# Optimization experiments

Measured on AMD Instinct MI355X. Metric: run time of the kernel, lower is better.

## Reference

```python
import jax, jax.numpy as jnp
import numpy as np

N_NODES = 100000
N_EDGES = 3200000
IN_F, HID_F, OUT_F = 6, 32, 3


def setup_inputs() -> dict:
    key = jax.random.key(0)
    k_feat, k_src, k_dst, k_w1, k_w2 = jax.random.split(key, 5)
    features = jax.random.normal(k_feat, (N_NODES, IN_F), dtype=jnp.float32)
    src = jax.random.randint(k_src, (N_EDGES,), 0, N_NODES, dtype=jnp.int32)
    dst = jax.random.randint(k_dst, (N_EDGES,), 0, N_NODES, dtype=jnp.int32)
    # Glorot-style weights for the two customConv layers
    W1 = jax.random.normal(k_w1, (IN_F, HID_F), dtype=jnp.float32) / np.sqrt(IN_F)
    b1 = jnp.zeros((HID_F,), dtype=jnp.float32)
    W2 = jax.random.normal(k_w2, (HID_F, OUT_F), dtype=jnp.float32) / np.sqrt(HID_F)
    b2 = jnp.zeros((OUT_F,), dtype=jnp.float32)
    return {"features": features, "src": src, "dst": dst,
            "W1": W1, "b1": b1, "W2": W2, "b2": b2}


def _custom_conv(src, dst, h, W, b):
    """DGL-GraphConv-style layer: mean-aggregate src->dst, then linear.
    h: [N, F_in]; returns [N, F_out]."""
    n = h.shape[0]
    # gather source features along edges, scatter-add to destinations
    msg_sum = jax.ops.segment_sum(h[src], dst, num_segments=n)  # [N, F_in]
    deg = jax.ops.segment_sum(jnp.ones_like(dst, dtype=h.dtype), dst,
                              num_segments=n)                    # [N]
    agg = msg_sum / jnp.maximum(deg, 1.0)[:, None]               # mean over in-neighbors
    return agg @ W + b


def reference(features, src, dst, W1, b1, W2, b2):
    x = _custom_conv(src, dst, features, W1, b1)  # [N, 32]
    x = jax.nn.relu(x)                            # activation inside customConv
    x = _custom_conv(src, dst, x, W2, b2)         # [N, 3]
    return x
```

## Files before the change

### kernel.cpp

```cpp
#include <hip/hip_runtime.h>


#define IN_F 6
#define HID_F 32
#define OUT_F 3

#define NPB 256
#define NPB_SHIFT 8
#define NBMAX 512
#define CAPB 9728
#define CHUNK 8192
#define SRC_BITS 17
#define SRC_MASK ((1u << SRC_BITS) - 1)

__global__ __launch_bounds__(1024)
void k_scatter(const int* __restrict__ src, const int* __restrict__ dst,
               int nB, int* __restrict__ cursor_g,
               unsigned* __restrict__ packed, int nE) {
    __shared__ int      hist[NBMAX];
    __shared__ int      base_l[NBMAX];
    __shared__ int      base_g[NBMAX];
    __shared__ int      cur[NBMAX];
    __shared__ unsigned sorted_l[CHUNK];
    __shared__ unsigned short bkt_l[CHUNK];

    const int tid = threadIdx.x;
    int e0 = blockIdx.x * CHUNK;
    int e1 = min(e0 + CHUNK, nE);
    int cnt = e1 - e0;

    for (int b = tid; b < nB; b += blockDim.x) hist[b] = 0;
    __syncthreads();

    for (int e = e0 + tid; e < e1; e += blockDim.x)
        atomicAdd(&hist[dst[e] >> NPB_SHIFT], 1);
    __syncthreads();

    if (tid < nB) base_l[tid] = hist[tid];
    __syncthreads();
    for (int off = 1; off < nB; off <<= 1) {
        int v = 0;
        if (tid < nB) {
            v = base_l[tid];
            if (tid >= off) v += base_l[tid - off];
        }
        __syncthreads();
        if (tid < nB) base_l[tid] = v;
        __syncthreads();
    }

    int h_r = 0, ex_r = 0;
    if (tid < nB) {
        h_r  = hist[tid];
        ex_r = base_l[tid] - h_r;
        base_g[tid] = h_r ? atomicAdd(&cursor_g[tid], h_r) : 0;
        cur[tid] = ex_r;
    }
    __syncthreads();
    if (tid < nB) base_l[tid] = ex_r;
    __syncthreads();

    for (int e = e0 + tid; e < e1; e += blockDim.x) {
        int d = dst[e];
        int b = d >> NPB_SHIFT;
        unsigned rec = ((unsigned)(d & (NPB - 1)) << SRC_BITS) | (unsigned)src[e];
        int p = atomicAdd(&cur[b], 1);
        sorted_l[p] = rec;
        bkt_l[p] = (unsigned short)b;
    }
    __syncthreads();

    for (int i = tid; i < cnt; i += blockDim.x) {
        int b = bkt_l[i];
        int rel = base_g[b] + (i - base_l[b]);
        if (rel < CAPB) packed[(size_t)b * CAPB + rel] = sorted_l[i];
    }
}

__global__ __launch_bounds__(1024)
void k_sort(unsigned* __restrict__ packed, const int* __restrict__ cursor_g,
            int* __restrict__ offv, int* __restrict__ cntv, int nN) {
    __shared__ int      hist[NPB];
    __shared__ int      base[NPB];
    __shared__ int      cur[NPB];
    __shared__ unsigned sorted[CAPB];

    const int tid = threadIdx.x;
    int b = blockIdx.x;
    int ecnt = min(cursor_g[b], CAPB);
    unsigned* ep = packed + (size_t)b * CAPB;

    if (tid < NPB) hist[tid] = 0;
    __syncthreads();

    for (int i = tid; i < ecnt; i += blockDim.x)
        atomicAdd(&hist[ep[i] >> SRC_BITS], 1);
    __syncthreads();

    if (tid < NPB) base[tid] = hist[tid];
    __syncthreads();
    for (int off = 1; off < NPB; off <<= 1) {
        int v = 0;
        if (tid < NPB) {
            v = base[tid];
            if (tid >= off) v += base[tid - off];
        }
        __syncthreads();
        if (tid < NPB) base[tid] = v;
        __syncthreads();
    }

    int n0 = b << NPB_SHIFT;
    int h_r = 0, ex_r = 0;
    if (tid < NPB) {
        h_r  = hist[tid];
        ex_r = base[tid] - h_r;
        cur[tid] = ex_r;
        int n = n0 + tid;
        if (n < nN) { offv[n] = b * CAPB + ex_r; cntv[n] = h_r; }
    }
    __syncthreads();
    if (tid < NPB) base[tid] = ex_r;
    __syncthreads();

    for (int i = tid; i < ecnt; i += blockDim.x) {
        unsigned p = ep[i];
        int dl = (int)(p >> SRC_BITS);
        int pos = atomicAdd(&cur[dl], 1);
        sorted[pos] = p & SRC_MASK;
    }
    __syncthreads();

    for (int i = tid; i < ecnt; i += blockDim.x) ep[i] = sorted[i];
}

__global__ void k_l1(const unsigned* __restrict__ csr, const int* __restrict__ offv,
                     const int* __restrict__ cntv, const float* __restrict__ feat,
                     const float* __restrict__ W1, const float* __restrict__ b1,
                     const float* __restrict__ W2, float4* __restrict__ g4, int nN) {
    __shared__ float sW1[IN_F * HID_F];
    __shared__ float sb1[HID_F];
    __shared__ float sW2[HID_F * OUT_F];
    for (int i = threadIdx.x; i < IN_F * HID_F; i += blockDim.x)  sW1[i] = W1[i];
    for (int i = threadIdx.x; i < HID_F; i += blockDim.x)         sb1[i] = b1[i];
    for (int i = threadIdx.x; i < HID_F * OUT_F; i += blockDim.x) sW2[i] = W2[i];
    __syncthreads();

    int n = blockIdx.x * blockDim.x + threadIdx.x;
    if (n >= nN) return;

    int off = offv[n], c = cntv[n];
    const unsigned* row = csr + off;

    float s0 = 0.f, s1 = 0.f, s2 = 0.f, s3 = 0.f, s4 = 0.f, s5 = 0.f;
#define ACC_FEAT(S)                                                        \
    do {                                                                   \
        const float* f = feat + (size_t)(S) * IN_F;                        \
        float2 f01 = *reinterpret_cast<const float2*>(f + 0);              \
        float2 f23 = *reinterpret_cast<const float2*>(f + 2);              \
        float2 f45 = *reinterpret_cast<const float2*>(f + 4);              \
        s0 += f01.x; s1 += f01.y; s2 += f23.x;                             \
        s3 += f23.y; s4 += f45.x; s5 += f45.y;                             \
    } while (0)

    int i = 0;
    for (; i + 4 <= c; i += 4) {
        unsigned a0 = row[i], a1 = row[i + 1], a2 = row[i + 2], a3 = row[i + 3];
        ACC_FEAT(a0); ACC_FEAT(a1); ACC_FEAT(a2); ACC_FEAT(a3);
    }
    for (; i < c; ++i) ACC_FEAT(row[i]);
#undef ACC_FEAT

    float inv = 1.0f / fmaxf((float)c, 1.0f);
    float a0 = s0 * inv, a1 = s1 * inv, a2 = s2 * inv;
    float a3 = s3 * inv, a4 = s4 * inv, a5 = s5 * inv;

    float g0 = 0.f, g1 = 0.f, g2 = 0.f;
#pragma unroll
    for (int j = 0; j < HID_F; ++j) {
        float t = sb1[j];
        t = fmaf(a0, sW1[0 * HID_F + j], t);
        t = fmaf(a1, sW1[1 * HID_F + j], t);
        t = fmaf(a2, sW1[2 * HID_F + j], t);
        t = fmaf(a3, sW1[3 * HID_F + j], t);
        t = fmaf(a4, sW1[4 * HID_F + j], t);
        t = fmaf(a5, sW1[5 * HID_F + j], t);
        t = fmaxf(t, 0.0f);
        g0 = fmaf(t, sW2[j * OUT_F + 0], g0);
        g1 = fmaf(t, sW2[j * OUT_F + 1], g1);
        g2 = fmaf(t, sW2[j * OUT_F + 2], g2);
    }
    g4[n] = make_float4(g0, g1, g2, 0.0f);
}

__global__ void k_l2(const unsigned* __restrict__ csr, const int* __restrict__ offv,
                     const int* __restrict__ cntv, const float4* __restrict__ g4,
                     const float* __restrict__ b2, float* __restrict__ out, int nN) {
    int n = blockIdx.x * blockDim.x + threadIdx.x;
    if (n >= nN) return;

    int off = offv[n], c = cntv[n];
    const unsigned* row = csr + off;

    float s0 = 0.f, s1 = 0.f, s2 = 0.f;
    int i = 0;
    for (; i + 4 <= c; i += 4) {
        unsigned a0 = row[i], a1 = row[i + 1], a2 = row[i + 2], a3 = row[i + 3];
        float4 ga = g4[a0], gb = g4[a1], gc = g4[a2], gd = g4[a3];
        s0 += ga.x + gb.x + gc.x + gd.x;
        s1 += ga.y + gb.y + gc.y + gd.y;
        s2 += ga.z + gb.z + gc.z + gd.z;
    }
    for (; i < c; ++i) {
        float4 ga = g4[row[i]];
        s0 += ga.x; s1 += ga.y; s2 += ga.z;
    }

    float inv = 1.0f / fmaxf((float)c, 1.0f);
    out[(size_t)n * OUT_F + 0] = s0 * inv + b2[0];
    out[(size_t)n * OUT_F + 1] = s1 * inv + b2[1];
    out[(size_t)n * OUT_F + 2] = s2 * inv + b2[2];
}

__global__ void scatter1(const int* __restrict__ src, const int* __restrict__ dst,
                         const float* __restrict__ feat,
                         float* __restrict__ acc1, float* __restrict__ deg, int nE) {
    int e = blockIdx.x * blockDim.x + threadIdx.x;
    if (e >= nE) return;
    int s = src[e], d = dst[e];
    const float* f = feat + (size_t)s * IN_F;
    float* a = acc1 + (size_t)d * IN_F;
    float2 f01 = *reinterpret_cast<const float2*>(f + 0);
    float2 f23 = *reinterpret_cast<const float2*>(f + 2);
    float2 f45 = *reinterpret_cast<const float2*>(f + 4);
    atomicAdd(a + 0, f01.x); atomicAdd(a + 1, f01.y); atomicAdd(a + 2, f23.x);
    atomicAdd(a + 3, f23.y); atomicAdd(a + 4, f45.x); atomicAdd(a + 5, f45.y);
    atomicAdd(deg + d, 1.0f);
}

__global__ void node_mlp(float* __restrict__ acc1, const float* __restrict__ deg,
                         const float* __restrict__ W1, const float* __restrict__ b1,
                         const float* __restrict__ W2, int nN) {
    __shared__ float sW1[IN_F * HID_F];
    __shared__ float sb1[HID_F];
    __shared__ float sW2[HID_F * OUT_F];
    for (int i = threadIdx.x; i < IN_F * HID_F; i += blockDim.x)  sW1[i] = W1[i];
    for (int i = threadIdx.x; i < HID_F; i += blockDim.x)         sb1[i] = b1[i];
    for (int i = threadIdx.x; i < HID_F * OUT_F; i += blockDim.x) sW2[i] = W2[i];
    __syncthreads();
    int n = blockIdx.x * blockDim.x + threadIdx.x;
    if (n >= nN) return;
    float inv = 1.0f / fmaxf(deg[n], 1.0f);
    float a[IN_F];
    float* row = acc1 + (size_t)n * IN_F;
#pragma unroll
    for (int i = 0; i < IN_F; ++i) a[i] = row[i] * inv;
    float g0 = 0.f, g1 = 0.f, g2 = 0.f;
#pragma unroll
    for (int j = 0; j < HID_F; ++j) {
        float t = sb1[j];
#pragma unroll
        for (int i = 0; i < IN_F; ++i) t = fmaf(a[i], sW1[i * HID_F + j], t);
        t = fmaxf(t, 0.0f);
        g0 = fmaf(t, sW2[j * OUT_F + 0], g0);
        g1 = fmaf(t, sW2[j * OUT_F + 1], g1);
        g2 = fmaf(t, sW2[j * OUT_F + 2], g2);
    }
    row[0] = g0; row[1] = g1; row[2] = g2;
}

__global__ void scatter2(const int* __restrict__ src, const int* __restrict__ dst,
                         const float* __restrict__ g, float* __restrict__ acc2, int nE) {
    int e = blockIdx.x * blockDim.x + threadIdx.x;
    if (e >= nE) return;
    int s = src[e], d = dst[e];
    const float* gs = g + (size_t)s * IN_F;
    float* a = acc2 + (size_t)d * OUT_F;
    float2 g01 = *reinterpret_cast<const float2*>(gs);
    atomicAdd(a + 0, g01.x); atomicAdd(a + 1, g01.y); atomicAdd(a + 2, gs[2]);
}

__global__ void finalize(const float* __restrict__ acc2, const float* __restrict__ deg,
                         const float* __restrict__ b2, float* __restrict__ out, int nN) {
    int n = blockIdx.x * blockDim.x + threadIdx.x;
    if (n >= nN) return;
    float inv = 1.0f / fmaxf(deg[n], 1.0f);
    out[(size_t)n * OUT_F + 0] = acc2[(size_t)n * OUT_F + 0] * inv + b2[0];
    out[(size_t)n * OUT_F + 1] = acc2[(size_t)n * OUT_F + 1] * inv + b2[1];
    out[(size_t)n * OUT_F + 2] = acc2[(size_t)n * OUT_F + 2] * inv + b2[2];
}

extern "C" void kernel_launch(void* const* d_in, const int* in_sizes, int n_in,
                              void* d_out, int out_size, void* d_ws, size_t ws_size,
                              hipStream_t stream) {
    const float* feat = (const float*)d_in[0];
    const int*   src  = (const int*)d_in[1];
    const int*   dst  = (const int*)d_in[2];
    const float* W1   = (const float*)d_in[3];
    const float* b1   = (const float*)d_in[4];
    const float* W2   = (const float*)d_in[5];
    const float* b2   = (const float*)d_in[6];
    float* out = (float*)d_out;

    const int nN = in_sizes[0] / IN_F;
    const int nE = in_sizes[1];

    int nB = (nN + NPB - 1) >> NPB_SHIFT;
    int nC = (nE + CHUNK - 1) / CHUNK;

    size_t off_g4     = 0;
    size_t off_offv   = off_g4 + (size_t)nN * sizeof(float4);
    size_t off_cntv   = off_offv + (size_t)nN * sizeof(int);
    size_t off_cursor = off_cntv + (size_t)nN * sizeof(int);
    size_t off_packed = (off_cursor + (size_t)nB * sizeof(int) + 255) & ~(size_t)255;
    size_t need_fast  = off_packed + (size_t)nB * CAPB * sizeof(unsigned);

    bool fast = (ws_size >= need_fast) &&
                (nN <= (int)(SRC_MASK + 1)) &&
                (nB <= NBMAX) &&
                (nE / nB <= CAPB - 1500);

    if (fast) {
        float4*   g4     = (float4*)((char*)d_ws + off_g4);
        int*      offv   = (int*)((char*)d_ws + off_offv);
        int*      cntv   = (int*)((char*)d_ws + off_cntv);
        int*      cursor = (int*)((char*)d_ws + off_cursor);
        unsigned* packed = (unsigned*)((char*)d_ws + off_packed);

        hipMemsetAsync(cursor, 0, (size_t)nB * sizeof(int), stream);
        k_scatter<<<nC, 1024, 0, stream>>>(src, dst, nB, cursor, packed, nE);
        k_sort<<<nB, 1024, 0, stream>>>(packed, cursor, offv, cntv, nN);
        k_l1<<<(nN + 255) / 256, 256, 0, stream>>>(packed, offv, cntv, feat,
                                                   W1, b1, W2, g4, nN);
        k_l2<<<(nN + 255) / 256, 256, 0, stream>>>(packed, offv, cntv, g4, b2, out, nN);
    } else {
        float* deg  = (float*)d_ws;
        float* acc1 = deg + nN;
        float* acc2 = acc1 + (size_t)nN * IN_F;
        const int TB = 256;
        int eblocks = (nE + TB - 1) / TB;
        int nblocks = (nN + TB - 1) / TB;
        hipMemsetAsync(d_ws, 0, (size_t)nN * 10 * sizeof(float), stream);
        scatter1<<<eblocks, TB, 0, stream>>>(src, dst, feat, acc1, deg, nE);
        node_mlp<<<nblocks, TB, 0, stream>>>(acc1, deg, W1, b1, W2, nN);
        scatter2<<<eblocks, TB, 0, stream>>>(src, dst, acc1, acc2, nE);
        finalize<<<nblocks, TB, 0, stream>>>(acc2, deg, b2, out, nN);
    }
}
```

Before: 92.95 us.

## Fuse layer-1 aggregation into sort kernel using shared-memory CSR

Merges the per-bucket sort kernel with the first-layer gather and MLP. The sorted source indices and per-node counts and offsets are reused directly from shared memory instead of being re-read from global memory in a separate kernel. Each node is handled by four lanes that split its edges and hidden units and combine results with xor shuffles. The cursor memset is also replaced by a tiny zeroing kernel. The cost is a longer sort kernel with more shared memory and register use, which may lower occupancy.

```diff
diff --git a/kernel.cpp b/kernel.cpp
--- a/kernel.cpp
+++ b/kernel.cpp
@@ -12,6 +12,10 @@
 #define CHUNK 8192
 #define SRC_BITS 17
 #define SRC_MASK ((1u << SRC_BITS) - 1)
+
+__global__ void k_zero(int* __restrict__ cursor, int nB) {
+    for (int i = threadIdx.x; i < nB; i += blockDim.x) cursor[i] = 0;
+}
 
 __global__ __launch_bounds__(1024)
 void k_scatter(const int* __restrict__ src, const int* __restrict__ dst,
@@ -78,18 +82,28 @@
 }
 
 __global__ __launch_bounds__(1024)
-void k_sort(unsigned* __restrict__ packed, const int* __restrict__ cursor_g,
-            int* __restrict__ offv, int* __restrict__ cntv, int nN) {
+void k_sl1(unsigned* __restrict__ packed, const int* __restrict__ cursor_g,
+           const float* __restrict__ feat,
+           const float* __restrict__ W1, const float* __restrict__ b1,
+           const float* __restrict__ W2,
+           float4* __restrict__ g4, int* __restrict__ offv, int* __restrict__ cntv,
+           int nN) {
     __shared__ int      hist[NPB];
     __shared__ int      base[NPB];
     __shared__ int      cur[NPB];
     __shared__ unsigned sorted[CAPB];
+    __shared__ float    sW1[IN_F * HID_F];
+    __shared__ float    sb1[HID_F];
+    __shared__ float    sW2[HID_F * OUT_F];
 
     const int tid = threadIdx.x;
     int b = blockIdx.x;
     int ecnt = min(cursor_g[b], CAPB);
     unsigned* ep = packed + (size_t)b * CAPB;
 
+    for (int i = tid; i < IN_F * HID_F; i += blockDim.x)  sW1[i] = W1[i];
+    for (int i = tid; i < HID_F; i += blockDim.x)         sb1[i] = b1[i];
+    for (int i = tid; i < HID_F * OUT_F; i += blockDim.x) sW2[i] = W2[i];
     if (tid < NPB) hist[tid] = 0;
     __syncthreads();
 
@@ -132,52 +146,41 @@
     __syncthreads();
 
     for (int i = tid; i < ecnt; i += blockDim.x) ep[i] = sorted[i];
-}
-
-__global__ void k_l1(const unsigned* __restrict__ csr, const int* __restrict__ offv,
-                     const int* __restrict__ cntv, const float* __restrict__ feat,
-                     const float* __restrict__ W1, const float* __restrict__ b1,
-                     const float* __restrict__ W2, float4* __restrict__ g4, int nN) {
-    __shared__ float sW1[IN_F * HID_F];
-    __shared__ float sb1[HID_F];
-    __shared__ float sW2[HID_F * OUT_F];
-    for (int i = threadIdx.x; i < IN_F * HID_F; i += blockDim.x)  sW1[i] = W1[i];
-    for (int i = threadIdx.x; i < HID_F; i += blockDim.x)         sb1[i] = b1[i];
-    for (int i = threadIdx.x; i < HID_F * OUT_F; i += blockDim.x) sW2[i] = W2[i];
-    __syncthreads();
-
-    int n = blockIdx.x * blockDim.x + threadIdx.x;
-    if (n >= nN) return;
-
-    int off = offv[n], c = cntv[n];
-    const unsigned* row = csr + off;
+
+    int node = tid >> 2;
+    int sub  = tid & 3;
+    int n    = n0 + node;
+    bool live = (n < nN);
 
     float s0 = 0.f, s1 = 0.f, s2 = 0.f, s3 = 0.f, s4 = 0.f, s5 = 0.f;
-#define ACC_FEAT(S)                                                        \
-    do {                                                                   \
-        const float* f = feat + (size_t)(S) * IN_F;                        \
-        float2 f01 = *reinterpret_cast<const float2*>(f + 0);              \
-        float2 f23 = *reinterpret_cast<const float2*>(f + 2);              \
-        float2 f45 = *reinterpret_cast<const float2*>(f + 4);              \
-        s0 += f01.x; s1 += f01.y; s2 += f23.x;                             \
-        s3 += f23.y; s4 += f45.x; s5 += f45.y;                             \
-    } while (0)
-
-    int i = 0;
-    for (; i + 4 <= c; i += 4) {
-        unsigned a0 = row[i], a1 = row[i + 1], a2 = row[i + 2], a3 = row[i + 3];
-        ACC_FEAT(a0); ACC_FEAT(a1); ACC_FEAT(a2); ACC_FEAT(a3);
-    }
-    for (; i < c; ++i) ACC_FEAT(row[i]);
-#undef ACC_FEAT
+    int st = 0, c = 0;
+    if (live) { st = base[node]; c = hist[node]; }
+
+    for (int i = st + sub; i < st + c; i += 4) {
+        unsigned s = sorted[i];
+        const float* f = feat + (size_t)s * IN_F;
+        float2 f01 = *reinterpret_cast<const float2*>(f + 0);
+        float2 f23 = *reinterpret_cast<const float2*>(f + 2);
+        float2 f45 = *reinterpret_cast<const float2*>(f + 4);
+        s0 += f01.x; s1 += f01.y; s2 += f23.x;
+        s3 += f23.y; s4 += f45.x; s5 += f45.y;
+    }
+    s0 += __shfl_xor(s0, 1); s0 += __shfl_xor(s0, 2);
+    s1 += __shfl_xor(s1, 1); s1 += __shfl_xor(s1, 2);
+    s2 += __shfl_xor(s2, 1); s2 += __shfl_xor(s2, 2);
+    s3 += __shfl_xor(s3, 1); s3 += __shfl_xor(s3, 2);
+    s4 += __shfl_xor(s4, 1); s4 += __shfl_xor(s4, 2);
+    s5 += __shfl_xor(s5, 1); s5 += __shfl_xor(s5, 2);
 
     float inv = 1.0f / fmaxf((float)c, 1.0f);
     float a0 = s0 * inv, a1 = s1 * inv, a2 = s2 * inv;
     float a3 = s3 * inv, a4 = s4 * inv, a5 = s5 * inv;
 
     float g0 = 0.f, g1 = 0.f, g2 = 0.f;
+    int j0 = sub * (HID_F / 4);
 #pragma unroll
-    for (int j = 0; j < HID_F; ++j) {
+    for (int jj = 0; jj < HID_F / 4; ++jj) {
+        int j = j0 + jj;
         float t = sb1[j];
         t = fmaf(a0, sW1[0 * HID_F + j], t);
         t = fmaf(a1, sW1[1 * HID_F + j], t);
@@ -190,7 +193,11 @@
         g1 = fmaf(t, sW2[j * OUT_F + 1], g1);
         g2 = fmaf(t, sW2[j * OUT_F + 2], g2);
     }
-    g4[n] = make_float4(g0, g1, g2, 0.0f);
+    g0 += __shfl_xor(g0, 1); g0 += __shfl_xor(g0, 2);
+    g1 += __shfl_xor(g1, 1); g1 += __shfl_xor(g1, 2);
+    g2 += __shfl_xor(g2, 1); g2 += __shfl_xor(g2, 2);
+
+    if (live && sub == 0) g4[n] = make_float4(g0, g1, g2, 0.0f);
 }
 
 __global__ void k_l2(const unsigned* __restrict__ csr, const int* __restrict__ offv,
@@ -327,11 +334,10 @@
         int*      cursor = (int*)((char*)d_ws + off_cursor);
         unsigned* packed = (unsigned*)((char*)d_ws + off_packed);
 
-        hipMemsetAsync(cursor, 0, (size_t)nB * sizeof(int), stream);
+        k_zero<<<1, 512, 0, stream>>>(cursor, nB);
         k_scatter<<<nC, 1024, 0, stream>>>(src, dst, nB, cursor, packed, nE);
-        k_sort<<<nB, 1024, 0, stream>>>(packed, cursor, offv, cntv, nN);
-        k_l1<<<(nN + 255) / 256, 256, 0, stream>>>(packed, offv, cntv, feat,
-                                                   W1, b1, W2, g4, nN);
+        k_sl1<<<nB, 1024, 0, stream>>>(packed, cursor, feat, W1, b1, W2,
+                                       g4, offv, cntv, nN);
         k_l2<<<(nN + 255) / 256, 256, 0, stream>>>(packed, offv, cntv, g4, b2, out, nN);
     } else {
         float* deg  = (float*)d_ws;
```

Result: faster. 78.63 us (-15.4%).
